# Kernel tuning notes

Measured on AMD Instinct MI355X. Metric: run time of the kernel, lower is better.

The kernel has to match this reference:

```python
import jax, jax.numpy as jnp
import numpy as np

D = 1024      # feature_dim / vertice_dim
H = 4         # n_heads
HD = D // H   # head dim 256
DFF = 2 * D   # 2048
DV = 1024     # vertice_dim
T = 64        # frame_num
PERIOD = 30
NEG = -1e9


def setup_inputs() -> dict:
    key = jax.random.key(0)
    ks = iter(jax.random.split(key, 32))
    sc = 0.02
    def w(shape):
        return jax.random.normal(next(ks), shape, dtype=jnp.float32) * sc
    return {
        "hidden_states": jax.random.normal(next(ks), (T, DV), dtype=jnp.float32),
        "hid_w": w((D, DV)), "hid_b": w((D,)),
        "obj_w": w((D, 80)),
        "sa_in_w": w((3 * D, D)), "sa_in_b": w((3 * D,)),
        "sa_out_w": w((D, D)), "sa_out_b": w((D,)),
        "ca_in_w": w((3 * D, D)), "ca_in_b": w((3 * D,)),
        "ca_out_w": w((D, D)), "ca_out_b": w((D,)),
        "ln1_g": jnp.ones((D,), jnp.float32), "ln1_b": jnp.zeros((D,), jnp.float32),
        "ln2_g": jnp.ones((D,), jnp.float32), "ln2_b": jnp.zeros((D,), jnp.float32),
        "ln3_g": jnp.ones((D,), jnp.float32), "ln3_b": jnp.zeros((D,), jnp.float32),
        "ff1_w": w((DFF, D)), "ff1_b": w((DFF,)),
        "ff2_w": w((D, DFF)), "ff2_b": w((D,)),
        "vr_w": w((DV, D)), "vr_b": w((DV,)),
        "vm_w": w((D, DV)), "vm_b": w((D,)),
    }


def _periodic_pe():
    # sin/cos PE over one period, tiled (PeriodicPositionalEncoding)
    pos = jnp.arange(PERIOD, dtype=jnp.float32)[:, None]
    div = jnp.exp(jnp.arange(0, D, 2, dtype=jnp.float32) * (-np.log(10000.0) / D))
    pe = jnp.zeros((PERIOD, D), jnp.float32)
    pe = pe.at[:, 0::2].set(jnp.sin(pos * div)).at[:, 1::2].set(jnp.cos(pos * div))
    reps = T // PERIOD + 1
    return jnp.tile(pe, (reps, 1))[:T]  # (T, D)


def reference(hidden_states, hid_w, hid_b, obj_w,
              sa_in_w, sa_in_b, sa_out_w, sa_out_b,
              ca_in_w, ca_in_b, ca_out_w, ca_out_b,
              ln1_g, ln1_b, ln2_g, ln2_b, ln3_g, ln3_b,
              ff1_w, ff1_b, ff2_w, ff2_b, vr_w, vr_b, vm_w, vm_b):
    mem = hidden_states @ hid_w.T + hid_b          # (S=T, D)
    style = obj_w[:, 0]                             # one-hot(0) @ obj_vector
    pe = _periodic_pe()

    # ALiBi-style biased causal mask (init_biased_mask, n_head=4)
    slopes = 0.25 ** jnp.arange(1, H + 1, dtype=jnp.float32)
    idx = jnp.arange(T)
    i_, j_ = idx[:, None], idx[None, :]
    alibi = -((i_ - j_) // PERIOD).astype(jnp.float32)
    tgt_bias = jnp.where(j_ <= i_, slopes[:, None, None] * alibi[None], NEG)  # (H,T,T)
    # vocaset enc_dec_mask: frame i may only attend memory frame i
    mem_bias = jnp.where(i_ == j_, 0.0, NEG)  # (T,S)

    def mha(q_in, kv_in, in_w, in_b, out_w, out_b, bias):
        wq, wk, wv = jnp.split(in_w, 3, axis=0)
        bq, bk, bv = jnp.split(in_b, 3)
        q = (q_in @ wq.T + bq).reshape(-1, H, HD)
        k = (kv_in @ wk.T + bk).reshape(-1, H, HD)
        v = (kv_in @ wv.T + bv).reshape(-1, H, HD)
        s = jnp.einsum('qhd,khd->hqk', q, k) / np.sqrt(HD) + bias
        a = jax.nn.softmax(s, axis=-1)
        o = jnp.einsum('hqk,khd->qhd', a, v).reshape(-1, D)
        return o @ out_w.T + out_b

    def ln(x, g, b):
        m = x.mean(-1, keepdims=True)
        v = ((x - m) ** 2).mean(-1, keepdims=True)
        return (x - m) / jnp.sqrt(v + 1e-5) * g + b

    def decode(x):  # post-norm TransformerDecoderLayer (eval, dropout off)
        x = ln(x + mha(x, x, sa_in_w, sa_in_b, sa_out_w, sa_out_b, tgt_bias), ln1_g, ln1_b)
        x = ln(x + mha(x, mem, ca_in_w, ca_in_b, ca_out_w, ca_out_b, mem_bias[None]), ln2_g, ln2_b)
        h = jax.nn.relu(x @ ff1_w.T + ff1_b) @ ff2_w.T + ff2_b
        return ln(x + h, ln3_g, ln3_b)

    # independent of the zero-padded future slots, matching the growing-seq loop.
    emb0 = jnp.zeros((T, D), jnp.float32).at[0].set(style)

    def step(emb, i):
        out = decode(emb + pe)
        new_tok = (out[i] @ vr_w.T + vr_b) @ vm_w.T + vm_b + style
        return emb.at[i + 1].set(new_tok), None

    emb, _ = jax.lax.scan(step, emb0, jnp.arange(T - 1))
    # final iteration's vertice_out over the full T-length sequence
    return decode(emb + pe) @ vr_w.T + vr_b  # (T, DV)
```

## Files before the change

### kernel.cpp

```cpp
#include <hip/hip_runtime.h>
#include <math.h>

#define DIM  1024
#define SEQ  64
#define HDIM 256
#define NBLK 256
#define SLOT_STRIDE 32
#define SENTU 0xFFC00ABCu

__device__ __forceinline__ float wsum(float v){
  v += __shfl_xor(v, 32, 64); v += __shfl_xor(v, 16, 64); v += __shfl_xor(v, 8, 64);
  v += __shfl_xor(v, 4, 64);  v += __shfl_xor(v, 2, 64);  v += __shfl_xor(v, 1, 64);
  return v;
}
__device__ __forceinline__ float wmax(float v){
  v = fmaxf(v, __shfl_xor(v, 32, 64)); v = fmaxf(v, __shfl_xor(v, 16, 64));
  v = fmaxf(v, __shfl_xor(v, 8, 64));  v = fmaxf(v, __shfl_xor(v, 4, 64));
  v = fmaxf(v, __shfl_xor(v, 2, 64));  v = fmaxf(v, __shfl_xor(v, 1, 64));
  return v;
}
__device__ __forceinline__ float2 breduce2(float va, float vb, float* red){
  int tid = threadIdx.x;
  va = wsum(va); vb = wsum(vb);
  if ((tid & 63) == 0){ red[(tid >> 6) * 2] = va; red[(tid >> 6) * 2 + 1] = vb; }
  __syncthreads();
  float ra = red[0] + red[2] + red[4] + red[6];
  float rb = red[1] + red[3] + red[5] + red[7];
  __syncthreads();
  return make_float2(ra, rb);
}

__device__ __forceinline__ float ldc(const float* p){
  return __hip_atomic_load(p, __ATOMIC_RELAXED, __HIP_MEMORY_SCOPE_AGENT);
}
__device__ __forceinline__ void stc(float* p, float v){
  __hip_atomic_store(p, v, __ATOMIC_RELAXED, __HIP_MEMORY_SCOPE_AGENT);
}
__device__ __forceinline__ float plc(const float* p){
  float v = ldc(p);
  unsigned s = 0;
  while (__float_as_uint(v) == SENTU){ v = ldc(p); if (++s > 200000000u) break; }
  return v;
}
__device__ __forceinline__ void poll4s(const float* p, int stride, float* out){
  float v0 = ldc(p), v1 = ldc(p + stride), v2 = ldc(p + 2 * stride), v3 = ldc(p + 3 * stride);
  unsigned s = 0;
  while (__float_as_uint(v0) == SENTU || __float_as_uint(v1) == SENTU ||
         __float_as_uint(v2) == SENTU || __float_as_uint(v3) == SENTU){
    v0 = ldc(p); v1 = ldc(p + stride); v2 = ldc(p + 2 * stride); v3 = ldc(p + 3 * stride);
    if (++s > 200000000u) break;
  }
  out[0] = v0; out[1] = v1; out[2] = v2; out[3] = v3;
}

__device__ __forceinline__ void spin_ge(unsigned* p, unsigned ep){
  unsigned spins = 0;
  while (__hip_atomic_load(p, __ATOMIC_RELAXED, __HIP_MEMORY_SCOPE_AGENT) < ep){
    if (++spins > 100000000u) break;
  }
}
__device__ __forceinline__ void gsync(unsigned* slots, unsigned ep, int bid, int tid){
  asm volatile("s_waitcnt vmcnt(0)" ::: "memory");
  __syncthreads();
  if (tid == 0)
    __hip_atomic_store(&slots[bid * SLOT_STRIDE], ep, __ATOMIC_RELAXED, __HIP_MEMORY_SCOPE_AGENT);
  spin_ge(&slots[tid * SLOT_STRIDE], ep);
  __syncthreads();
  asm volatile("" ::: "memory");
}

__global__ void mm1024(const float* __restrict__ A0, const float* __restrict__ B,
                       float* __restrict__ C0, size_t Astride, size_t Cstride){
  const float* A = A0 + (size_t)blockIdx.z * Astride;
  float* C = C0 + (size_t)blockIdx.z * Cstride;
  __shared__ float As[16][65];
  __shared__ float Bs[16][65];
  int ta = blockIdx.y * 64, tb = blockIdx.x * 64;
  int tx = threadIdx.x & 15, ty = threadIdx.x >> 4;
  float acc[4][4] = {};
  for (int k0 = 0; k0 < 1024; k0 += 16){
    #pragma unroll
    for (int j = 0; j < 4; ++j)
      As[tx][ty * 4 + j] = A[(size_t)(ta + ty * 4 + j) * 1024 + k0 + tx];
    {
      const float4 bv = *(const float4*)&B[(size_t)(k0 + ty) * 1024 + tb + tx * 4];
      Bs[ty][tx * 4]     = bv.x; Bs[ty][tx * 4 + 1] = bv.y;
      Bs[ty][tx * 4 + 2] = bv.z; Bs[ty][tx * 4 + 3] = bv.w;
    }
    __syncthreads();
    #pragma unroll
    for (int kk = 0; kk < 16; ++kk){
      float av[4], bv[4];
      #pragma unroll
      for (int m = 0; m < 4; ++m) av[m] = As[kk][ty * 4 + m];
      #pragma unroll
      for (int n = 0; n < 4; ++n) bv[n] = Bs[kk][tx * 4 + n];
      #pragma unroll
      for (int m = 0; m < 4; ++m)
        #pragma unroll
        for (int n = 0; n < 4; ++n) acc[m][n] = fmaf(av[m], bv[n], acc[m][n]);
    }
    __syncthreads();
  }
  #pragma unroll
  for (int m = 0; m < 4; ++m){
    float4 ov = { acc[m][0], acc[m][1], acc[m][2], acc[m][3] };
    *(float4*)&C[(size_t)(ta + ty * 4 + m) * 1024 + tb + tx * 4] = ov;
  }
}

__global__ void sentinit(unsigned* p, size_t n){
  size_t idx = (size_t)blockIdx.x * 256 + threadIdx.x;
  for (size_t k = idx; k < n; k += (size_t)gridDim.x * 256) p[k] = SENTU;
}

struct CoopArgs {
  const float *hs, *hid_w, *hid_b;
  const float *sa_in_w, *sa_in_b, *sa_out_w, *sa_out_b;
  const float *ca_in_w, *ca_in_b, *ca_out_w, *ca_out_b;
  const float *ln1_g, *ln1_b, *ln2_g, *ln2_b, *ln3_g, *ln3_b;
  const float *ff1_w, *ff1_b, *ff2_w, *ff2_b;
  const float *vr_w, *vr_b, *vm_w, *vm_b, *obj_w;
  const float *Cm, *WqF, *WkF, *WvF;
  float *mem, *vtmp, *cac;
  float *kc, *qv, *vcB, *uB, *hbB, *wB, *sB;
  float *peT, *stylev, *cbvec, *wqpeT, *wkpeT, *wvpeT;
  float *out;
  unsigned *bar;
};

__global__ void __launch_bounds__(256, 2) decode_loop(CoopArgs a){
  const int tid = threadIdx.x, bid = blockIdx.x;
  const int wave = tid >> 6, lane = tid & 63;
  const int gw = bid * 4 + wave;
  __shared__ float smA[2048];
  __shared__ float smB[1024];
  __shared__ float scp[256];
  __shared__ float red[8];
  unsigned bep = 0;
  const float NLOG = -9.210340371976184f / 1024.0f;

  {
    float pw[16];
    const float* pr = a.hid_w + (size_t)gw * DIM;
    #pragma unroll
    for (int k = 0; k < 16; ++k) pw[k] = pr[lane + 64 * k];
    float bias = a.hid_b[gw];
    for (int t = 0; t < 64; ++t){
      const float* xr = a.hs + (size_t)t * DIM;
      float acc = 0.f;
      #pragma unroll
      for (int k = 0; k < 16; ++k) acc = fmaf(pw[k], xr[lane + 64 * k], acc);
      acc = wsum(acc);
      if (lane == 0) stc(a.mem + (size_t)t * DIM + gw, acc + bias);
    }
    if (bid < 30){
      int p = bid;
      for (int d = tid; d < DIM; d += 256){
        float dv = __expf((float)(2 * (d >> 1)) * NLOG);
        float arg = (float)p * dv;
        stc(a.peT + (size_t)p * DIM + d, (d & 1) ? cosf(arg) : sinf(arg));
      }
    } else if (bid == 30){
      for (int d = tid; d < DIM; d += 256) stc(a.stylev + d, a.obj_w[(size_t)d * 80]);
    }
  }
  ++bep; gsync(a.bar, bep, bid, tid);

  float cbv;
  {
    const float* pv = a.vm_w + (size_t)gw * DIM;
    float acc = 0.f;
    #pragma unroll
    for (int k = 0; k < 16; ++k) acc = fmaf(pv[lane + 64 * k], a.vr_b[lane + 64 * k], acc);
    acc = wsum(acc);
    cbv = acc + a.vm_b[gw] + ldc(a.stylev + gw);
    if (lane == 0) stc(a.cbvec + gw, cbv);
  }
  {
    float pw[16];
    const float* pr = a.ca_in_w + (size_t)(2 * DIM + gw) * DIM;
    #pragma unroll
    for (int k = 0; k < 16; ++k) pw[k] = pr[lane + 64 * k];
    float bias = a.ca_in_b[2 * DIM + gw];
    for (int t = 0; t < 64; ++t){
      const float* xr = a.mem + (size_t)t * DIM;
      #pragma unroll
      for (int k = 0; k < 4; ++k) smA[tid + 256 * k] = ldc(xr + tid + 256 * k);
      __syncthreads();
      float acc = 0.f;
      #pragma unroll
      for (int k = 0; k < 16; ++k) acc = fmaf(pw[k], smA[lane + 64 * k], acc);
      acc = wsum(acc);
      if (lane == 0) stc(a.vtmp + (size_t)t * DIM + gw, acc + bias);
      __syncthreads();
    }
  }
  ++bep; gsync(a.bar, bep, bid, tid);

  {
    float pw[16];
    const float* pr = a.ca_out_w + (size_t)gw * DIM;
    #pragma unroll
    for (int k = 0; k < 16; ++k) pw[k] = pr[lane + 64 * k];
    float bias = a.ca_out_b[gw];
    for (int t = 0; t < 64; ++t){
      const float* xr = a.vtmp + (size_t)t * DIM;
      #pragma unroll
      for (int k = 0; k < 4; ++k) smA[tid + 256 * k] = ldc(xr + tid + 256 * k);
      __syncthreads();
      float acc = 0.f;
      #pragma unroll
      for (int k = 0; k < 16; ++k) acc = fmaf(pw[k], smA[lane + 64 * k], acc);
      acc = wsum(acc);
      if (lane == 0) stc(a.cac + (size_t)t * DIM + gw, acc + bias);
      __syncthreads();
    }
  }
  ++bep; gsync(a.bar, bep, bid, tid);

  float aqcb, akcb, avcb;
  {
    float wqr[16], wkr[16], wvr[16];
    const float* pq = a.sa_in_w + (size_t)gw * DIM;
    const float* pk = a.sa_in_w + (size_t)(DIM + gw) * DIM;
    const float* pv = a.sa_in_w + (size_t)(2 * DIM + gw) * DIM;
    #pragma unroll
    for (int k = 0; k < 16; ++k){
      int d = lane + 64 * k;
      wqr[k] = pq[d]; wkr[k] = pk[d]; wvr[k] = pv[d];
    }
    const float b_q = a.sa_in_b[gw];
    const float b_k = a.sa_in_b[DIM + gw];
    const float b_v = a.sa_in_b[2 * DIM + gw];
    float dq = 0.f, dk = 0.f, dv = 0.f, sq = 0.f, sk = 0.f, sv = 0.f;
    #pragma unroll
    for (int k = 0; k < 16; ++k){
      float xc = ldc(a.cbvec + lane + 64 * k);
      float xs = ldc(a.stylev + lane + 64 * k);
      dq = fmaf(wqr[k], xc, dq); dk = fmaf(wkr[k], xc, dk); dv = fmaf(wvr[k], xc, dv);
      sq = fmaf(wqr[k], xs, sq); sk = fmaf(wkr[k], xs, sk); sv = fmaf(wvr[k], xs, sv);
    }
    aqcb = wsum(dq) + b_q; akcb = wsum(dk) + b_k; avcb = wsum(dv) + b_v;
    sq = wsum(sq); sk = wsum(sk); sv = wsum(sv);
    float pq0 = 0.f, pk0 = 0.f, pv0 = 0.f;
    for (int p = 0; p < 30; ++p){
      const float* pp = a.peT + (size_t)p * DIM;
      float tq = 0.f, tk = 0.f, tv = 0.f;
      #pragma unroll
      for (int k = 0; k < 16; ++k){
        float x = ldc(pp + lane + 64 * k);
        tq = fmaf(wqr[k], x, tq); tk = fmaf(wkr[k], x, tk); tv = fmaf(wvr[k], x, tv);
      }
      tq = wsum(tq); tk = wsum(tk); tv = wsum(tv);
      if (lane == 0){
        stc(a.wqpeT + (size_t)p * DIM + gw, tq);
        stc(a.wkpeT + (size_t)p * DIM + gw, tk);
        stc(a.wvpeT + (size_t)p * DIM + gw, tv);
      }
      if (p == 0){ pq0 = tq; pk0 = tk; pv0 = tv; }
    }
    if (lane == 0){
      stc(a.qv + gw, sq + pq0 + b_q);
      stc(a.kc + gw, sk + pk0 + b_k);
      stc(a.vcB + gw, sv + pv0 + b_v);
    }
  }
  ++bep; gsync(a.bar, bep, bid, tid);

  float fq[16], fk[16], fv[16], wo[16], f1a[16], f1b[16], f2[32];
  {
    const float* pq = a.WqF + (size_t)gw * DIM;
    const float* pk = a.WkF + (size_t)gw * DIM;
    const float* pv = a.WvF + (size_t)gw * DIM;
    const float* po = a.sa_out_w + (size_t)gw * DIM;
    const float* p1a = a.ff1_w + (size_t)(2 * gw) * DIM;
    const float* p1b = a.ff1_w + (size_t)(2 * gw + 1) * DIM;
    const float* p2 = a.ff2_w + (size_t)gw * 2048;
    #pragma unroll
    for (int k = 0; k < 16; ++k){
      int d = lane + 64 * k;
      fq[k] = pq[d]; fk[k] = pk[d]; fv[k] = pv[d]; wo[k] = po[d];
      f1a[k] = p1a[d]; f1b[k] = p1b[d];
    }
    #pragma unroll
    for (int k = 0; k < 32; ++k) f2[k] = p2[lane + 64 * k];
  }
  const float b_o  = a.sa_out_b[gw];
  const float b_1a = a.ff1_b[2 * gw];
  const float b_1b = a.ff1_b[2 * gw + 1];
  const float b_2  = a.ff2_b[gw];
  const float b_vr = a.vr_b[gw];

  float c0 = 0.f, c1 = 0.f, c2 = 0.f, c3 = 0.f;
  const bool is_score = (bid < 16);
  const int sc_h  = bid >> 2;
  const int sc_jg = bid & 3;
  const float sc_slope = 1.0f / (float)(4 << (2 * sc_h));

  float xres = a.obj_w[(size_t)gw * 80] + ldc(a.peT + gw);
  float vrr[16], cmr[16];

  for (int i = 0; i < SEQ; ++i){
    {
      float vv[4];
      poll4s(a.vcB + (size_t)i * DIM + tid, 256, vv);
      smB[tid] = vv[0]; smB[tid + 256] = vv[1]; smB[tid + 512] = vv[2]; smB[tid + 768] = vv[3];
      __syncthreads();
      float p0 = 0.f, p1 = 0.f, p2 = 0.f, p3 = 0.f;
      #pragma unroll
      for (int k = 0; k < 4; ++k){
        p0 = fmaf(wo[k],      smB[lane + 64 * k],        p0);
        p1 = fmaf(wo[k + 4],  smB[lane + 64 * (k + 4)],  p1);
        p2 = fmaf(wo[k + 8],  smB[lane + 64 * (k + 8)],  p2);
        p3 = fmaf(wo[k + 12], smB[lane + 64 * (k + 12)], p3);
      }
      p0 = wsum(p0); p1 = wsum(p1); p2 = wsum(p2); p3 = wsum(p3);
      if (lane == i){ c0 = p0; c1 = p1; c2 = p2; c3 = p3; }
      if (is_score){
        float q4[4];
        poll4s(a.qv + (size_t)i * DIM + sc_h * HDIM + lane, 64, q4);
        #pragma unroll
        for (int jj = 0; jj < 4; ++jj){
          int j = sc_jg * 16 + wave * 4 + jj;
          if (j <= i){
            const float* kr = a.kc + (size_t)j * DIM + sc_h * HDIM + lane;
            float acc = 0.f;
            #pragma unroll
            for (int m = 0; m < 4; ++m) acc = fmaf(q4[m], plc(kr + m * 64), acc);
            acc = wsum(acc);
            if (lane == 0)
              stc(a.sB + (size_t)i * 256 + sc_h * 64 + j,
                  acc * 0.0625f - sc_slope * (float)((i - j) / 30));
          }
        }
      }
      float sv = (lane <= i) ? plc(a.sB + (size_t)i * 256 + wave * 64 + lane) : -3.0e38f;
      float mx = wmax(sv);
      float p = (lane <= i) ? __expf(sv - mx) : 0.f;
      float sum = wsum(p);
      scp[wave * 64 + lane] = p / sum;
      __syncthreads();
      float t = scp[lane] * c0 + scp[64 + lane] * c1 + scp[128 + lane] * c2 + scp[192 + lane] * c3;
      t = wsum(t);
      if (lane == 0) stc(a.uB + (size_t)i * DIM + gw, xres + t + b_o);
      __syncthreads();
    }

    float x2v;
    {
      float cr[4];
      #pragma unroll
      for (int k = 0; k < 4; ++k) cr[k] = ldc(a.cac + (size_t)i * DIM + tid + 256 * k);
      float uv[4];
      poll4s(a.uB + (size_t)i * DIM + tid, 256, uv);
      smA[tid] = uv[0]; smA[tid + 256] = uv[1]; smA[tid + 512] = uv[2]; smA[tid + 768] = uv[3];
      __syncthreads();
      float sa = 0.f, sb = 0.f;
      #pragma unroll
      for (int k = 0; k < 4; ++k){ float x = smA[tid + 256 * k]; sa += x; sb = fmaf(x, x, sb); }
      float2 r = breduce2(sa, sb, red);
      float mean = r.x * (1.f / 1024.f);
      float var  = r.y * (1.f / 1024.f) - mean * mean;
      float rs = 1.f / sqrtf(var + 1e-5f);
      float tv[4];
      float ta = 0.f, tb = 0.f;
      #pragma unroll
      for (int k = 0; k < 4; ++k){
        int d = tid + 256 * k;
        float x1 = (smA[d] - mean) * rs * a.ln1_g[d] + a.ln1_b[d];
        tv[k] = x1 + cr[k];
        ta += tv[k]; tb = fmaf(tv[k], tv[k], tb);
      }
      float2 r2v = breduce2(ta, tb, red);
      float mean2 = r2v.x * (1.f / 1024.f);
      float var2  = r2v.y * (1.f / 1024.f) - mean2 * mean2;
      float rs2 = 1.f / sqrtf(var2 + 1e-5f);
      #pragma unroll
      for (int k = 0; k < 4; ++k){
        int d = tid + 256 * k;
        smA[d] = (tv[k] - mean2) * rs2 * a.ln2_g[d] + a.ln2_b[d];
      }
      __syncthreads();
      x2v = smA[gw];
      float acc0 = 0.f, acc1 = 0.f;
      #pragma unroll
      for (int k = 0; k < 16; ++k){
        float x = smA[lane + 64 * k];
        acc0 = fmaf(f1a[k], x, acc0);
        acc1 = fmaf(f1b[k], x, acc1);
      }
      acc0 = wsum(acc0); acc1 = wsum(acc1);
      if (lane == 0){
        stc(a.hbB + (size_t)i * 2048 + 2 * gw,     fmaxf(acc0 + b_1a, 0.f));
        stc(a.hbB + (size_t)i * 2048 + 2 * gw + 1, fmaxf(acc1 + b_1b, 0.f));
      }
      __syncthreads();
    }

    {
      const float* pr = a.vr_w + (size_t)gw * DIM;
      const float* pc = a.Cm + (size_t)gw * DIM;
      #pragma unroll
      for (int k = 0; k < 16; ++k){ vrr[k] = pr[lane + 64 * k]; cmr[k] = pc[lane + 64 * k]; }
      float h0[4], h1[4];
      poll4s(a.hbB + (size_t)i * 2048 + tid, 256, h0);
      poll4s(a.hbB + (size_t)i * 2048 + 1024 + tid, 256, h1);
      #pragma unroll
      for (int k = 0; k < 4; ++k){ smA[tid + 256 * k] = h0[k]; smA[tid + 1024 + 256 * k] = h1[k]; }
      __syncthreads();
      float acc = 0.f;
      #pragma unroll
      for (int k = 0; k < 32; ++k) acc = fmaf(f2[k], smA[lane + 64 * k], acc);
      acc = wsum(acc);
      if (lane == 0) stc(a.wB + (size_t)i * DIM + gw, x2v + acc + b_2);
      __syncthreads();
    }

    {
      float wv4[4];
      poll4s(a.wB + (size_t)i * DIM + tid, 256, wv4);
      smA[tid] = wv4[0]; smA[tid + 256] = wv4[1]; smA[tid + 512] = wv4[2]; smA[tid + 768] = wv4[3];
      __syncthreads();
      float sa = 0.f, sb = 0.f;
      #pragma unroll
      for (int k = 0; k < 4; ++k){ float x = smA[tid + 256 * k]; sa += x; sb = fmaf(x, x, sb); }
      float2 r = breduce2(sa, sb, red);
      float mean = r.x * (1.f / 1024.f);
      float var  = r.y * (1.f / 1024.f) - mean * mean;
      float rs = 1.f / sqrtf(var + 1e-5f);
      float ov[4];
      #pragma unroll
      for (int k = 0; k < 4; ++k){
        int d = tid + 256 * k;
        ov[k] = (smA[d] - mean) * rs * a.ln3_g[d] + a.ln3_b[d];
      }
      __syncthreads();
      #pragma unroll
      for (int k = 0; k < 4; ++k) smA[tid + 256 * k] = ov[k];
      __syncthreads();
      float ar = 0.f, ac = 0.f, aqn = 0.f, akn = 0.f, avn = 0.f;
      #pragma unroll
      for (int k = 0; k < 16; ++k){
        float x = smA[lane + 64 * k];
        ar  = fmaf(vrr[k], x, ar);
        ac  = fmaf(cmr[k], x, ac);
        aqn = fmaf(fq[k], x, aqn);
        akn = fmaf(fk[k], x, akn);
        avn = fmaf(fv[k], x, avn);
      }
      ar = wsum(ar); ac = wsum(ac);
      aqn = wsum(aqn); akn = wsum(akn); avn = wsum(avn);
      if (lane == 0) a.out[(size_t)i * DIM + gw] = ar + b_vr;
      if (i < SEQ - 1){
        int pn = (i + 1) % 30;
        if (lane == 0){
          float tq = ldc(a.wqpeT + (size_t)pn * DIM + gw);
          float tk = ldc(a.wkpeT + (size_t)pn * DIM + gw);
          float tv = ldc(a.wvpeT + (size_t)pn * DIM + gw);
          stc(a.qv + (size_t)(i + 1) * DIM + gw, aqn + aqcb + tq);
          stc(a.kc + (size_t)(i + 1) * DIM + gw, akn + akcb + tk);
          stc(a.vcB + (size_t)(i + 1) * DIM + gw, avn + avcb + tv);
        }
        xres = ac + cbv + ldc(a.peT + (size_t)pn * DIM + gw);
      }
      __syncthreads();
    }
  }
}

extern "C" void kernel_launch(void* const* d_in, const int* in_sizes, int n_in,
                              void* d_out, int out_size, void* d_ws, size_t ws_size,
                              hipStream_t stream){
  const float* hs       = (const float*)d_in[0];
  const float* hid_w    = (const float*)d_in[1];
  const float* hid_b    = (const float*)d_in[2];
  const float* obj_w    = (const float*)d_in[3];
  const float* sa_in_w  = (const float*)d_in[4];
  const float* sa_in_b  = (const float*)d_in[5];
  const float* sa_out_w = (const float*)d_in[6];
  const float* sa_out_b = (const float*)d_in[7];
  const float* ca_in_w  = (const float*)d_in[8];
  const float* ca_in_b  = (const float*)d_in[9];
  const float* ca_out_w = (const float*)d_in[10];
  const float* ca_out_b = (const float*)d_in[11];
  const float* ln1_g    = (const float*)d_in[12];
  const float* ln1_b    = (const float*)d_in[13];
  const float* ln2_g    = (const float*)d_in[14];
  const float* ln2_b    = (const float*)d_in[15];
  const float* ln3_g    = (const float*)d_in[16];
  const float* ln3_b    = (const float*)d_in[17];
  const float* ff1_w    = (const float*)d_in[18];
  const float* ff1_b    = (const float*)d_in[19];
  const float* ff2_w    = (const float*)d_in[20];
  const float* ff2_b    = (const float*)d_in[21];
  const float* vr_w     = (const float*)d_in[22];
  const float* vr_b     = (const float*)d_in[23];
  const float* vm_w     = (const float*)d_in[24];
  const float* vm_b     = (const float*)d_in[25];

  float* ws = (float*)d_ws;
  float* mem    = ws;
  float* vtmp   = ws + 65536;
  float* cac    = ws + 131072;
  float* kc     = ws + 196608;
  float* qv     = ws + 262144;
  float* vcB    = ws + 327680;
  float* uB     = ws + 393216;
  float* hbB    = ws + 458752;
  float* wB     = ws + 589824;
  float* sB     = ws + 655360;
  float* peT    = ws + 671744;
  float* stylev = ws + 702464;
  float* cbvec  = ws + 703488;
  float* wqpeT  = ws + 704512;
  float* wkpeT  = ws + 735232;
  float* wvpeT  = ws + 765952;
  unsigned* bar = (unsigned*)(ws + 796672);
  float* Cm     = ws + 804864;
  float* WqF    = ws + 1853440;
  float* WkF    = ws + 2902016;
  float* WvF    = ws + 3950592;

  hipMemsetAsync((void*)bar, 0, 256 * SLOT_STRIDE * 4, stream);
  sentinit<<<512, 256, 0, stream>>>((unsigned*)kc, 475136);

  mm1024<<<dim3(16, 16, 1), 256, 0, stream>>>(vm_w, vr_w, Cm, 0, 0);
  mm1024<<<dim3(16, 16, 3), 256, 0, stream>>>(sa_in_w, Cm, WqF,
                                              (size_t)1024 * 1024, (size_t)1024 * 1024);

  CoopArgs A;
  A.hs = hs; A.hid_w = hid_w; A.hid_b = hid_b;
  A.sa_in_w = sa_in_w; A.sa_in_b = sa_in_b; A.sa_out_w = sa_out_w; A.sa_out_b = sa_out_b;
  A.ca_in_w = ca_in_w; A.ca_in_b = ca_in_b; A.ca_out_w = ca_out_w; A.ca_out_b = ca_out_b;
  A.ln1_g = ln1_g; A.ln1_b = ln1_b; A.ln2_g = ln2_g; A.ln2_b = ln2_b; A.ln3_g = ln3_g; A.ln3_b = ln3_b;
  A.ff1_w = ff1_w; A.ff1_b = ff1_b; A.ff2_w = ff2_w; A.ff2_b = ff2_b;
  A.vr_w = vr_w; A.vr_b = vr_b; A.vm_w = vm_w; A.vm_b = vm_b; A.obj_w = obj_w;
  A.Cm = Cm; A.WqF = WqF; A.WkF = WkF; A.WvF = WvF;
  A.mem = mem; A.vtmp = vtmp; A.cac = cac;
  A.kc = kc; A.qv = qv; A.vcB = vcB; A.uB = uB; A.hbB = hbB; A.wB = wB; A.sB = sB;
  A.peT = peT; A.stylev = stylev; A.cbvec = cbvec;
  A.wqpeT = wqpeT; A.wkpeT = wkpeT; A.wvpeT = wvpeT;
  A.out = (float*)d_out;
  A.bar = bar;

  void* params[1] = { &A };
  hipError_t e = hipLaunchCooperativeKernel((void*)decode_loop, dim3(NBLK), dim3(256), params, 0, stream);
  if (e != hipSuccess){
    decode_loop<<<dim3(NBLK), dim3(256), 0, stream>>>(A);
  }
}
```

Measured before the change: 2.049 ms.

## Repartition persistent decode kernel into 64 blocks of 1024 threads

Changes the cooperative persistent kernel from 256 blocks of 256 threads to 64 blocks of 1024 threads, so each block holds 16 waves and each thread owns one element of the 1024-wide vector. This cuts the number of participants in every grid barrier and in the sentinel polling of shared buffers, and simplifies the per-thread LayerNorm and load code. Attention scoring is remapped to one block per head, with the query staged in shared memory. The cost is heavier intra-block syncthreads, only 64 CUs in use with one block each, and larger block-level reductions.

```diff
diff --git a/kernel.cpp b/kernel.cpp
--- a/kernel.cpp
+++ b/kernel.cpp
@@ -4,7 +4,8 @@
 #define DIM  1024
 #define SEQ  64
 #define HDIM 256
-#define NBLK 256
+#define NBLK 64
+#define TPB  1024
 #define SLOT_STRIDE 32
 #define SENTU 0xFFC00ABCu
 
@@ -24,8 +25,9 @@
   va = wsum(va); vb = wsum(vb);
   if ((tid & 63) == 0){ red[(tid >> 6) * 2] = va; red[(tid >> 6) * 2 + 1] = vb; }
   __syncthreads();
-  float ra = red[0] + red[2] + red[4] + red[6];
-  float rb = red[1] + red[3] + red[5] + red[7];
+  float ra = 0.f, rb = 0.f;
+  #pragma unroll
+  for (int w = 0; w < 16; ++w){ ra += red[2 * w]; rb += red[2 * w + 1]; }
   __syncthreads();
   return make_float2(ra, rb);
 }
@@ -34,6 +36,9 @@
   return __hip_atomic_load(p, __ATOMIC_RELAXED, __HIP_MEMORY_SCOPE_AGENT);
 }
 __device__ __forceinline__ void stc(float* p, float v){
+  __hip_atomic_store(p, v, __ATOMIC_RELAXED, __HIP_MEMORY_SCOPE_AGENT);
+}
+__device__ __forceinline__ void sta(unsigned* p, unsigned v){
   __hip_atomic_store(p, v, __ATOMIC_RELAXED, __HIP_MEMORY_SCOPE_AGENT);
 }
 __device__ __forceinline__ float plc(const float* p){
@@ -42,17 +47,6 @@
   while (__float_as_uint(v) == SENTU){ v = ldc(p); if (++s > 200000000u) break; }
   return v;
 }
-__device__ __forceinline__ void poll4s(const float* p, int stride, float* out){
-  float v0 = ldc(p), v1 = ldc(p + stride), v2 = ldc(p + 2 * stride), v3 = ldc(p + 3 * stride);
-  unsigned s = 0;
-  while (__float_as_uint(v0) == SENTU || __float_as_uint(v1) == SENTU ||
-         __float_as_uint(v2) == SENTU || __float_as_uint(v3) == SENTU){
-    v0 = ldc(p); v1 = ldc(p + stride); v2 = ldc(p + 2 * stride); v3 = ldc(p + 3 * stride);
-    if (++s > 200000000u) break;
-  }
-  out[0] = v0; out[1] = v1; out[2] = v2; out[3] = v3;
-}
-
 __device__ __forceinline__ void spin_ge(unsigned* p, unsigned ep){
   unsigned spins = 0;
   while (__hip_atomic_load(p, __ATOMIC_RELAXED, __HIP_MEMORY_SCOPE_AGENT) < ep){
@@ -62,9 +56,8 @@
 __device__ __forceinline__ void gsync(unsigned* slots, unsigned ep, int bid, int tid){
   asm volatile("s_waitcnt vmcnt(0)" ::: "memory");
   __syncthreads();
-  if (tid == 0)
-    __hip_atomic_store(&slots[bid * SLOT_STRIDE], ep, __ATOMIC_RELAXED, __HIP_MEMORY_SCOPE_AGENT);
-  spin_ge(&slots[tid * SLOT_STRIDE], ep);
+  if (tid == 0) sta(&slots[bid * SLOT_STRIDE], ep);
+  if (tid < NBLK) spin_ge(&slots[tid * SLOT_STRIDE], ep);
   __syncthreads();
   asm volatile("" ::: "memory");
 }
@@ -129,14 +122,15 @@
   unsigned *bar;
 };
 
-__global__ void __launch_bounds__(256, 2) decode_loop(CoopArgs a){
+__global__ void __launch_bounds__(1024, 1) decode_loop(CoopArgs a){
   const int tid = threadIdx.x, bid = blockIdx.x;
   const int wave = tid >> 6, lane = tid & 63;
-  const int gw = bid * 4 + wave;
+  const int gw = bid * 16 + wave;
   __shared__ float smA[2048];
   __shared__ float smB[1024];
+  __shared__ float smC[256];
   __shared__ float scp[256];
-  __shared__ float red[8];
+  __shared__ float red[32];
   unsigned bep = 0;
   const float NLOG = -9.210340371976184f / 1024.0f;
 
@@ -156,13 +150,11 @@
     }
     if (bid < 30){
       int p = bid;
-      for (int d = tid; d < DIM; d += 256){
-        float dv = __expf((float)(2 * (d >> 1)) * NLOG);
-        float arg = (float)p * dv;
-        stc(a.peT + (size_t)p * DIM + d, (d & 1) ? cosf(arg) : sinf(arg));
-      }
+      float dv = __expf((float)(2 * (tid >> 1)) * NLOG);
+      float arg = (float)p * dv;
+      stc(a.peT + (size_t)p * DIM + tid, (tid & 1) ? cosf(arg) : sinf(arg));
     } else if (bid == 30){
-      for (int d = tid; d < DIM; d += 256) stc(a.stylev + d, a.obj_w[(size_t)d * 80]);
+      stc(a.stylev + tid, a.obj_w[(size_t)tid * 80]);
     }
   }
   ++bep; gsync(a.bar, bep, bid, tid);
@@ -184,9 +176,7 @@
     for (int k = 0; k < 16; ++k) pw[k] = pr[lane + 64 * k];
     float bias = a.ca_in_b[2 * DIM + gw];
     for (int t = 0; t < 64; ++t){
-      const float* xr = a.mem + (size_t)t * DIM;
-      #pragma unroll
-      for (int k = 0; k < 4; ++k) smA[tid + 256 * k] = ldc(xr + tid + 256 * k);
+      smA[tid] = ldc(a.mem + (size_t)t * DIM + tid);
       __syncthreads();
       float acc = 0.f;
       #pragma unroll
@@ -205,9 +195,7 @@
     for (int k = 0; k < 16; ++k) pw[k] = pr[lane + 64 * k];
     float bias = a.ca_out_b[gw];
     for (int t = 0; t < 64; ++t){
-      const float* xr = a.vtmp + (size_t)t * DIM;
-      #pragma unroll
-      for (int k = 0; k < 4; ++k) smA[tid + 256 * k] = ldc(xr + tid + 256 * k);
+      smA[tid] = ldc(a.vtmp + (size_t)t * DIM + tid);
       __syncthreads();
       float acc = 0.f;
       #pragma unroll
@@ -293,19 +281,16 @@
   const float b_vr = a.vr_b[gw];
 
   float c0 = 0.f, c1 = 0.f, c2 = 0.f, c3 = 0.f;
-  const bool is_score = (bid < 16);
-  const int sc_h  = bid >> 2;
-  const int sc_jg = bid & 3;
-  const float sc_slope = 1.0f / (float)(4 << (2 * sc_h));
+  const bool is_score = (bid < 4);
+  const float sc_slope = 1.0f / (float)(4 << (2 * bid));
 
   float xres = a.obj_w[(size_t)gw * 80] + ldc(a.peT + gw);
   float vrr[16], cmr[16];
 
   for (int i = 0; i < SEQ; ++i){
     {
-      float vv[4];
-      poll4s(a.vcB + (size_t)i * DIM + tid, 256, vv);
-      smB[tid] = vv[0]; smB[tid + 256] = vv[1]; smB[tid + 512] = vv[2]; smB[tid + 768] = vv[3];
+      smB[tid] = plc(a.vcB + (size_t)i * DIM + tid);
+      if (is_score && tid < 256) smC[tid] = plc(a.qv + (size_t)i * DIM + bid * HDIM + tid);
       __syncthreads();
       float p0 = 0.f, p1 = 0.f, p2 = 0.f, p3 = 0.f;
       #pragma unroll
@@ -318,28 +303,33 @@
       p0 = wsum(p0); p1 = wsum(p1); p2 = wsum(p2); p3 = wsum(p3);
       if (lane == i){ c0 = p0; c1 = p1; c2 = p2; c3 = p3; }
       if (is_score){
-        float q4[4];
-        poll4s(a.qv + (size_t)i * DIM + sc_h * HDIM + lane, 64, q4);
         #pragma unroll
         for (int jj = 0; jj < 4; ++jj){
-          int j = sc_jg * 16 + wave * 4 + jj;
+          int j = wave * 4 + jj;
           if (j <= i){
-            const float* kr = a.kc + (size_t)j * DIM + sc_h * HDIM + lane;
+            const float* kr = a.kc + (size_t)j * DIM + bid * HDIM + lane;
             float acc = 0.f;
             #pragma unroll
-            for (int m = 0; m < 4; ++m) acc = fmaf(q4[m], plc(kr + m * 64), acc);
+            for (int m = 0; m < 4; ++m) acc = fmaf(smC[m * 64 + lane], plc(kr + m * 64), acc);
             acc = wsum(acc);
             if (lane == 0)
-              stc(a.sB + (size_t)i * 256 + sc_h * 64 + j,
+              stc(a.sB + (size_t)i * 256 + bid * 64 + j,
                   acc * 0.0625f - sc_slope * (float)((i - j) / 30));
           }
         }
       }
-      float sv = (lane <= i) ? plc(a.sB + (size_t)i * 256 + wave * 64 + lane) : -3.0e38f;
-      float mx = wmax(sv);
-      float p = (lane <= i) ? __expf(sv - mx) : 0.f;
-      float sum = wsum(p);
-      scp[wave * 64 + lane] = p / sum;
+      if (tid < 256){
+        int j = tid & 63;
+        scp[tid] = (j <= i) ? plc(a.sB + (size_t)i * 256 + tid) : -3.0e38f;
+      }
+      __syncthreads();
+      if (wave < 4){
+        float sv = scp[wave * 64 + lane];
+        float mx = wmax(sv);
+        float p = (lane <= i) ? __expf(sv - mx) : 0.f;
+        float sum = wsum(p);
+        scp[wave * 64 + lane] = p / sum;
+      }
       __syncthreads();
       float t = scp[lane] * c0 + scp[64 + lane] * c1 + scp[128 + lane] * c2 + scp[192 + lane] * c3;
       t = wsum(t);
@@ -349,38 +339,19 @@
 
     float x2v;
     {
-      float cr[4];
-      #pragma unroll
-      for (int k = 0; k < 4; ++k) cr[k] = ldc(a.cac + (size_t)i * DIM + tid + 256 * k);
-      float uv[4];
-      poll4s(a.uB + (size_t)i * DIM + tid, 256, uv);
-      smA[tid] = uv[0]; smA[tid + 256] = uv[1]; smA[tid + 512] = uv[2]; smA[tid + 768] = uv[3];
-      __syncthreads();
-      float sa = 0.f, sb = 0.f;
-      #pragma unroll
-      for (int k = 0; k < 4; ++k){ float x = smA[tid + 256 * k]; sa += x; sb = fmaf(x, x, sb); }
-      float2 r = breduce2(sa, sb, red);
+      float cr = ldc(a.cac + (size_t)i * DIM + tid);
+      float xv = plc(a.uB + (size_t)i * DIM + tid);
+      float2 r = breduce2(xv, xv * xv, red);
       float mean = r.x * (1.f / 1024.f);
       float var  = r.y * (1.f / 1024.f) - mean * mean;
       float rs = 1.f / sqrtf(var + 1e-5f);
-      float tv[4];
-      float ta = 0.f, tb = 0.f;
-      #pragma unroll
-      for (int k = 0; k < 4; ++k){
-        int d = tid + 256 * k;
-        float x1 = (smA[d] - mean) * rs * a.ln1_g[d] + a.ln1_b[d];
-        tv[k] = x1 + cr[k];
-        ta += tv[k]; tb = fmaf(tv[k], tv[k], tb);
-      }
-      float2 r2v = breduce2(ta, tb, red);
+      float x1 = (xv - mean) * rs * a.ln1_g[tid] + a.ln1_b[tid];
+      float tv = x1 + cr;
+      float2 r2v = breduce2(tv, tv * tv, red);
       float mean2 = r2v.x * (1.f / 1024.f);
       float var2  = r2v.y * (1.f / 1024.f) - mean2 * mean2;
       float rs2 = 1.f / sqrtf(var2 + 1e-5f);
-      #pragma unroll
-      for (int k = 0; k < 4; ++k){
-        int d = tid + 256 * k;
-        smA[d] = (tv[k] - mean2) * rs2 * a.ln2_g[d] + a.ln2_b[d];
-      }
+      smA[tid] = (tv - mean2) * rs2 * a.ln2_g[tid] + a.ln2_b[tid];
       __syncthreads();
       x2v = smA[gw];
       float acc0 = 0.f, acc1 = 0.f;
@@ -403,11 +374,8 @@
       const float* pc = a.Cm + (size_t)gw * DIM;
       #pragma unroll
       for (int k = 0; k < 16; ++k){ vrr[k] = pr[lane + 64 * k]; cmr[k] = pc[lane + 64 * k]; }
-      float h0[4], h1[4];
-      poll4s(a.hbB + (size_t)i * 2048 + tid, 256, h0);
-      poll4s(a.hbB + (size_t)i * 2048 + 1024 + tid, 256, h1);
-      #pragma unroll
-      for (int k = 0; k < 4; ++k){ smA[tid + 256 * k] = h0[k]; smA[tid + 1024 + 256 * k] = h1[k]; }
+      smA[tid] = plc(a.hbB + (size_t)i * 2048 + tid);
+      smA[1024 + tid] = plc(a.hbB + (size_t)i * 2048 + 1024 + tid);
       __syncthreads();
       float acc = 0.f;
       #pragma unroll
@@ -418,26 +386,12 @@
     }
 
     {
-      float wv4[4];
-      poll4s(a.wB + (size_t)i * DIM + tid, 256, wv4);
-      smA[tid] = wv4[0]; smA[tid + 256] = wv4[1]; smA[tid + 512] = wv4[2]; smA[tid + 768] = wv4[3];
-      __syncthreads();
-      float sa = 0.f, sb = 0.f;
-      #pragma unroll
-      for (int k = 0; k < 4; ++k){ float x = smA[tid + 256 * k]; sa += x; sb = fmaf(x, x, sb); }
-      float2 r = breduce2(sa, sb, red);
+      float wvv = plc(a.wB + (size_t)i * DIM + tid);
+      float2 r = breduce2(wvv, wvv * wvv, red);
       float mean = r.x * (1.f / 1024.f);
       float var  = r.y * (1.f / 1024.f) - mean * mean;
       float rs = 1.f / sqrtf(var + 1e-5f);
-      float ov[4];
-      #pragma unroll
-      for (int k = 0; k < 4; ++k){
-        int d = tid + 256 * k;
-        ov[k] = (smA[d] - mean) * rs * a.ln3_g[d] + a.ln3_b[d];
-      }
-      __syncthreads();
-      #pragma unroll
-      for (int k = 0; k < 4; ++k) smA[tid + 256 * k] = ov[k];
+      smA[tid] = (wvv - mean) * rs * a.ln3_g[tid] + a.ln3_b[tid];
       __syncthreads();
       float ar = 0.f, ac = 0.f, aqn = 0.f, akn = 0.f, avn = 0.f;
       #pragma unroll
@@ -522,7 +476,7 @@
   float* WkF    = ws + 2902016;
   float* WvF    = ws + 3950592;
 
-  hipMemsetAsync((void*)bar, 0, 256 * SLOT_STRIDE * 4, stream);
+  hipMemsetAsync((void*)bar, 0, NBLK * SLOT_STRIDE * 4, stream);
   sentinit<<<512, 256, 0, stream>>>((unsigned*)kc, 475136);
 
   mm1024<<<dim3(16, 16, 1), 256, 0, stream>>>(vm_w, vr_w, Cm, 0, 0);
@@ -545,8 +499,8 @@
   A.bar = bar;
 
   void* params[1] = { &A };
-  hipError_t e = hipLaunchCooperativeKernel((void*)decode_loop, dim3(NBLK), dim3(256), params, 0, stream);
+  hipError_t e = hipLaunchCooperativeKernel((void*)decode_loop, dim3(NBLK), dim3(TPB), params, 0, stream);
   if (e != hipSuccess){
-    decode_loop<<<dim3(NBLK), dim3(256), 0, stream>>>(A);
-  }
-}
+    decode_loop<<<dim3(NBLK), dim3(TPB), 0, stream>>>(A);
+  }
+}
```

Result: slower. 3.819 ms (+86.3%).

## Compute attention scores redundantly per block instead of via global score buffer

Applied to the files above, without the earlier changes.

Each block now loads the full query row into shared memory and computes all head scores for the keys it needs, writing them to shared scratch instead of a global sB buffer. Score work is no longer limited to 16 blocks, so the cross-block publish/poll round trip on sB in every autoregressive step goes away. In exchange every block repeats the key dot products and reads the whole K cache each step, which adds memory traffic and compute.

```diff
diff --git a/kernel.cpp b/kernel.cpp
--- a/kernel.cpp
+++ b/kernel.cpp
@@ -5,6 +5,7 @@
 #define SEQ  64
 #define HDIM 256
 #define NBLK 256
+#define TPB  256
 #define SLOT_STRIDE 32
 #define SENTU 0xFFC00ABCu
 
@@ -36,11 +37,8 @@
 __device__ __forceinline__ void stc(float* p, float v){
   __hip_atomic_store(p, v, __ATOMIC_RELAXED, __HIP_MEMORY_SCOPE_AGENT);
 }
-__device__ __forceinline__ float plc(const float* p){
-  float v = ldc(p);
-  unsigned s = 0;
-  while (__float_as_uint(v) == SENTU){ v = ldc(p); if (++s > 200000000u) break; }
-  return v;
+__device__ __forceinline__ void sta(unsigned* p, unsigned v){
+  __hip_atomic_store(p, v, __ATOMIC_RELAXED, __HIP_MEMORY_SCOPE_AGENT);
 }
 __device__ __forceinline__ void poll4s(const float* p, int stride, float* out){
   float v0 = ldc(p), v1 = ldc(p + stride), v2 = ldc(p + 2 * stride), v3 = ldc(p + 3 * stride);
@@ -52,7 +50,18 @@
   }
   out[0] = v0; out[1] = v1; out[2] = v2; out[3] = v3;
 }
-
+__device__ __forceinline__ void poll8s(const float* p, float* out){
+  unsigned s = 0;
+  for (;;){
+    bool ok = true;
+    #pragma unroll
+    for (int m = 0; m < 8; ++m){ out[m] = ldc(p + 64 * m); }
+    #pragma unroll
+    for (int m = 0; m < 8; ++m) ok = ok && (__float_as_uint(out[m]) != SENTU);
+    if (ok) return;
+    if (++s > 50000000u) return;
+  }
+}
 __device__ __forceinline__ void spin_ge(unsigned* p, unsigned ep){
   unsigned spins = 0;
   while (__hip_atomic_load(p, __ATOMIC_RELAXED, __HIP_MEMORY_SCOPE_AGENT) < ep){
@@ -62,8 +71,7 @@
 __device__ __forceinline__ void gsync(unsigned* slots, unsigned ep, int bid, int tid){
   asm volatile("s_waitcnt vmcnt(0)" ::: "memory");
   __syncthreads();
-  if (tid == 0)
-    __hip_atomic_store(&slots[bid * SLOT_STRIDE], ep, __ATOMIC_RELAXED, __HIP_MEMORY_SCOPE_AGENT);
+  if (tid == 0) sta(&slots[bid * SLOT_STRIDE], ep);
   spin_ge(&slots[tid * SLOT_STRIDE], ep);
   __syncthreads();
   asm volatile("" ::: "memory");
@@ -123,7 +131,7 @@
   const float *vr_w, *vr_b, *vm_w, *vm_b, *obj_w;
   const float *Cm, *WqF, *WkF, *WvF;
   float *mem, *vtmp, *cac;
-  float *kc, *qv, *vcB, *uB, *hbB, *wB, *sB;
+  float *kc, *qv, *vcB, *uB, *hbB, *wB;
   float *peT, *stylev, *cbvec, *wqpeT, *wkpeT, *wvpeT;
   float *out;
   unsigned *bar;
@@ -135,6 +143,7 @@
   const int gw = bid * 4 + wave;
   __shared__ float smA[2048];
   __shared__ float smB[1024];
+  __shared__ float smC[1024];
   __shared__ float scp[256];
   __shared__ float red[8];
   unsigned bep = 0;
@@ -184,9 +193,8 @@
     for (int k = 0; k < 16; ++k) pw[k] = pr[lane + 64 * k];
     float bias = a.ca_in_b[2 * DIM + gw];
     for (int t = 0; t < 64; ++t){
-      const float* xr = a.mem + (size_t)t * DIM;
-      #pragma unroll
-      for (int k = 0; k < 4; ++k) smA[tid + 256 * k] = ldc(xr + tid + 256 * k);
+      #pragma unroll
+      for (int k = 0; k < 4; ++k) smA[tid + 256 * k] = ldc(a.mem + (size_t)t * DIM + tid + 256 * k);
       __syncthreads();
       float acc = 0.f;
       #pragma unroll
@@ -205,9 +213,8 @@
     for (int k = 0; k < 16; ++k) pw[k] = pr[lane + 64 * k];
     float bias = a.ca_out_b[gw];
     for (int t = 0; t < 64; ++t){
-      const float* xr = a.vtmp + (size_t)t * DIM;
-      #pragma unroll
-      for (int k = 0; k < 4; ++k) smA[tid + 256 * k] = ldc(xr + tid + 256 * k);
+      #pragma unroll
+      for (int k = 0; k < 4; ++k) smA[tid + 256 * k] = ldc(a.vtmp + (size_t)t * DIM + tid + 256 * k);
       __syncthreads();
       float acc = 0.f;
       #pragma unroll
@@ -293,19 +300,16 @@
   const float b_vr = a.vr_b[gw];
 
   float c0 = 0.f, c1 = 0.f, c2 = 0.f, c3 = 0.f;
-  const bool is_score = (bid < 16);
-  const int sc_h  = bid >> 2;
-  const int sc_jg = bid & 3;
-  const float sc_slope = 1.0f / (float)(4 << (2 * sc_h));
-
   float xres = a.obj_w[(size_t)gw * 80] + ldc(a.peT + gw);
   float vrr[16], cmr[16];
 
   for (int i = 0; i < SEQ; ++i){
     {
-      float vv[4];
+      float vv[4], qq[4];
       poll4s(a.vcB + (size_t)i * DIM + tid, 256, vv);
+      poll4s(a.qv + (size_t)i * DIM + tid, 256, qq);
       smB[tid] = vv[0]; smB[tid + 256] = vv[1]; smB[tid + 512] = vv[2]; smB[tid + 768] = vv[3];
+      smC[tid] = qq[0]; smC[tid + 256] = qq[1]; smC[tid + 512] = qq[2]; smC[tid + 768] = qq[3];
       __syncthreads();
       float p0 = 0.f, p1 = 0.f, p2 = 0.f, p3 = 0.f;
       #pragma unroll
@@ -317,29 +321,39 @@
       }
       p0 = wsum(p0); p1 = wsum(p1); p2 = wsum(p2); p3 = wsum(p3);
       if (lane == i){ c0 = p0; c1 = p1; c2 = p2; c3 = p3; }
-      if (is_score){
-        float q4[4];
-        poll4s(a.qv + (size_t)i * DIM + sc_h * HDIM + lane, 64, q4);
+      for (int j = wave; j <= i; j += 4){
+        const float* kr = a.kc + (size_t)j * DIM + lane;
+        float kv[8];
+        float s0 = 0.f, s1 = 0.f, s2 = 0.f, s3 = 0.f;
+        poll8s(kr, kv);
         #pragma unroll
-        for (int jj = 0; jj < 4; ++jj){
-          int j = sc_jg * 16 + wave * 4 + jj;
-          if (j <= i){
-            const float* kr = a.kc + (size_t)j * DIM + sc_h * HDIM + lane;
-            float acc = 0.f;
-            #pragma unroll
-            for (int m = 0; m < 4; ++m) acc = fmaf(q4[m], plc(kr + m * 64), acc);
-            acc = wsum(acc);
-            if (lane == 0)
-              stc(a.sB + (size_t)i * 256 + sc_h * 64 + j,
-                  acc * 0.0625f - sc_slope * (float)((i - j) / 30));
-          }
+        for (int mm = 0; mm < 4; ++mm){
+          s0 = fmaf(smC[lane + 64 * mm],       kv[mm],     s0);
+          s1 = fmaf(smC[256 + lane + 64 * mm], kv[4 + mm], s1);
         }
-      }
-      float sv = (lane <= i) ? plc(a.sB + (size_t)i * 256 + wave * 64 + lane) : -3.0e38f;
-      float mx = wmax(sv);
-      float p = (lane <= i) ? __expf(sv - mx) : 0.f;
-      float sum = wsum(p);
-      scp[wave * 64 + lane] = p / sum;
+        poll8s(kr + 512, kv);
+        #pragma unroll
+        for (int mm = 0; mm < 4; ++mm){
+          s2 = fmaf(smC[512 + lane + 64 * mm], kv[mm],     s2);
+          s3 = fmaf(smC[768 + lane + 64 * mm], kv[4 + mm], s3);
+        }
+        s0 = wsum(s0); s1 = wsum(s1); s2 = wsum(s2); s3 = wsum(s3);
+        if (lane == 0){
+          float ab = (float)((i - j) / 30);
+          scp[j]       = s0 * 0.0625f - 0.25f       * ab;
+          scp[64 + j]  = s1 * 0.0625f - 0.0625f     * ab;
+          scp[128 + j] = s2 * 0.0625f - 0.015625f   * ab;
+          scp[192 + j] = s3 * 0.0625f - 0.00390625f * ab;
+        }
+      }
+      __syncthreads();
+      {
+        float sv = (lane <= i) ? scp[wave * 64 + lane] : -3.0e38f;
+        float mx = wmax(sv);
+        float p = (lane <= i) ? __expf(sv - mx) : 0.f;
+        float sum = wsum(p);
+        scp[wave * 64 + lane] = p / sum;
+      }
       __syncthreads();
       float t = scp[lane] * c0 + scp[64 + lane] * c1 + scp[128 + lane] * c2 + scp[192 + lane] * c3;
       t = wsum(t);
@@ -509,21 +523,20 @@
   float* uB     = ws + 393216;
   float* hbB    = ws + 458752;
   float* wB     = ws + 589824;
-  float* sB     = ws + 655360;
-  float* peT    = ws + 671744;
-  float* stylev = ws + 702464;
-  float* cbvec  = ws + 703488;
-  float* wqpeT  = ws + 704512;
-  float* wkpeT  = ws + 735232;
-  float* wvpeT  = ws + 765952;
-  unsigned* bar = (unsigned*)(ws + 796672);
-  float* Cm     = ws + 804864;
-  float* WqF    = ws + 1853440;
-  float* WkF    = ws + 2902016;
-  float* WvF    = ws + 3950592;
+  float* peT    = ws + 655360;
+  float* stylev = ws + 686080;
+  float* cbvec  = ws + 687104;
+  float* wqpeT  = ws + 688128;
+  float* wkpeT  = ws + 718848;
+  float* wvpeT  = ws + 749568;
+  unsigned* bar = (unsigned*)(ws + 780288);
+  float* Cm     = ws + 788480;
+  float* WqF    = ws + 1837056;
+  float* WkF    = ws + 2885632;
+  float* WvF    = ws + 3934208;
 
   hipMemsetAsync((void*)bar, 0, 256 * SLOT_STRIDE * 4, stream);
-  sentinit<<<512, 256, 0, stream>>>((unsigned*)kc, 475136);
+  sentinit<<<512, 256, 0, stream>>>((unsigned*)kc, 458752);
 
   mm1024<<<dim3(16, 16, 1), 256, 0, stream>>>(vm_w, vr_w, Cm, 0, 0);
   mm1024<<<dim3(16, 16, 3), 256, 0, stream>>>(sa_in_w, Cm, WqF,
@@ -538,15 +551,15 @@
   A.vr_w = vr_w; A.vr_b = vr_b; A.vm_w = vm_w; A.vm_b = vm_b; A.obj_w = obj_w;
   A.Cm = Cm; A.WqF = WqF; A.WkF = WkF; A.WvF = WvF;
   A.mem = mem; A.vtmp = vtmp; A.cac = cac;
-  A.kc = kc; A.qv = qv; A.vcB = vcB; A.uB = uB; A.hbB = hbB; A.wB = wB; A.sB = sB;
+  A.kc = kc; A.qv = qv; A.vcB = vcB; A.uB = uB; A.hbB = hbB; A.wB = wB;
   A.peT = peT; A.stylev = stylev; A.cbvec = cbvec;
   A.wqpeT = wqpeT; A.wkpeT = wkpeT; A.wvpeT = wvpeT;
   A.out = (float*)d_out;
   A.bar = bar;
 
   void* params[1] = { &A };
-  hipError_t e = hipLaunchCooperativeKernel((void*)decode_loop, dim3(NBLK), dim3(256), params, 0, stream);
+  hipError_t e = hipLaunchCooperativeKernel((void*)decode_loop, dim3(NBLK), dim3(TPB), params, 0, stream);
   if (e != hipSuccess){
-    decode_loop<<<dim3(NBLK), dim3(256), 0, stream>>>(A);
-  }
-}
+    decode_loop<<<dim3(NBLK), dim3(TPB), 0, stream>>>(A);
+  }
+}
```

New measurement: 2.029 ms. No clear change (-1.0%).
